# Kernel optimization log

Measured on AMD Instinct MI355X. Metric: run time of the kernel, lower is better.

Reference implementation:

```python
import jax, jax.numpy as jnp
import numpy as np

B, T, D = 4, 2048, 1024
E, H, K = 8, 2048, 2  # n_expert, expert_dim, top_k


def setup_inputs() -> dict:
    key = jax.random.key(0)
    k1, k2, k3, k4 = jax.random.split(key, 4)
    x = jax.random.normal(k1, (B, T, D), jnp.float32)
    gate_w = jax.random.normal(k2, (D, E), jnp.float32) * 0.02          # Router gate (no bias)
    w1 = jax.random.normal(k3, (E, D, H), jnp.float32) * (1.0 / np.sqrt(D))  # per-expert first Linear
    w2 = jax.random.normal(k4, (E, H, D), jnp.float32) * (1.0 / np.sqrt(H))  # per-expert second Linear
    return {"x": x, "gate_w": gate_w, "w1": w1, "w2": w2}


def reference(x, gate_w, w1, w2):
    b, t, d = x.shape
    xf = x.reshape(-1, d)                                   # [N, D]
    n = xf.shape[0]
    n_expert = gate_w.shape[1]
    # Router
    logits = xf @ gate_w                                    # [N, E]
    probs = jax.nn.softmax(logits, axis=-1)
    topk_probs, topk_idx = jax.lax.top_k(probs, K)          # [N, K]
    topk_probs = topk_probs / jnp.sum(topk_probs, axis=-1, keepdims=True)
    # Dense compute of ALL experts (faithful to original), then gather top-k
    h = jax.nn.gelu(jnp.einsum('nd,edh->neh', xf, w1), approximate=False)  # [N, E, H]
    all_expert_out = jnp.einsum('neh,ehd->ned', h, w2)      # [N, E, D]
    selected = jnp.take_along_axis(all_expert_out, topk_idx[:, :, None], axis=1)  # [N, K, D]
    out = jnp.sum(topk_probs[:, :, None] * selected, axis=1)  # [N, D]  (dropout p=0 -> identity)
    # Load-balancing aux loss
    counts = jnp.zeros((n_expert,), jnp.float32).at[topk_idx.reshape(-1)].add(1.0)
    tokens_per_expert = counts / n
    mean_probs = jnp.mean(probs, axis=0)
    aux_loss = n_expert * jnp.sum(tokens_per_expert * mean_probs)
    return (out.reshape(b, t, d), aux_loss,
            probs.reshape(b, t, n_expert),
            topk_idx.reshape(b, t, K),
            topk_probs.reshape(b, t, K))
```

## Files before the change

kernel.cpp:

```cpp
#include <hip/hip_runtime.h>
#include <hip/hip_bf16.h>
#include <cstdint>

typedef unsigned short u16;
typedef unsigned int u32;
typedef short s16x8 __attribute__((ext_vector_type(8)));
typedef float f32x4 __attribute__((ext_vector_type(4)));

constexpr int NTOK = 8192;
constexpr int DDIM = 1024;
constexpr int NEXP = 8;
constexpr int HDIM = 2048;
constexpr int NPAIR = NTOK * 2;

constexpr size_t OFF_OUT   = 0;
constexpr size_t OFF_AUX   = 8388608;
constexpr size_t OFF_PROBS = 8388609;
constexpr size_t OFF_TIDX  = 8454145;
constexpr size_t OFF_TPR   = 8470529;

constexpr size_t WS_CNT  = 0;
constexpr size_t WS_PSUM = 32;
constexpr size_t WS_BASE = 64;
constexpr size_t WS_IDS  = 1024;
constexpr size_t WS_PRW  = 263168;
constexpr size_t WS_XB   = 525312;
constexpr size_t WS_W1T  = 17302528;
constexpr size_t WS_W2T  = 50856960;
constexpr size_t WS_H    = 84411392;
constexpr size_t WS_XG   = 151520256;
constexpr size_t WS_NEED = 185074688;

__device__ __forceinline__ u16 f2b(float f) {
  u32 u = __float_as_uint(f);
  u32 r = (u + 0x7fffu + ((u >> 16) & 1u)) >> 16;
  return (u16)r;
}

typedef const uint32_t __attribute__((address_space(1)))* gptr_t;
typedef uint32_t __attribute__((address_space(3)))* lptr_t;

__device__ __forceinline__ void gload16(const void* gp, void* lp) {
  __builtin_amdgcn_global_load_lds((gptr_t)gp, (lptr_t)(uintptr_t)lp, 16, 0, 0);
}

__global__ __launch_bounds__(256) void tconv_kernel(const float* __restrict__ in,
                                                    u16* __restrict__ out, int R, int C) {
  __shared__ float tile[64][65];
  int e = blockIdx.z;
  int c0 = blockIdx.x * 64, r0 = blockIdx.y * 64;
  int tx = threadIdx.x & 15, ty = threadIdx.x >> 4;
  const float* src = in + (size_t)e * R * C;
#pragma unroll
  for (int i = 0; i < 4; ++i) {
    int r = ty + i * 16;
    float4 v = *(const float4*)(src + (size_t)(r0 + r) * C + c0 + tx * 4);
    tile[r][tx * 4 + 0] = v.x; tile[r][tx * 4 + 1] = v.y;
    tile[r][tx * 4 + 2] = v.z; tile[r][tx * 4 + 3] = v.w;
  }
  __syncthreads();
  u16* dst = out + (size_t)e * R * C;
#pragma unroll
  for (int i = 0; i < 4; ++i) {
    int c = ty + i * 16;
    ushort4 o;
    o.x = f2b(tile[tx * 4 + 0][c]); o.y = f2b(tile[tx * 4 + 1][c]);
    o.z = f2b(tile[tx * 4 + 2][c]); o.w = f2b(tile[tx * 4 + 3][c]);
    *(ushort4*)(dst + (size_t)(c0 + c) * R + r0 + tx * 4) = o;
  }
}

__global__ __launch_bounds__(256) void router_kernel(
    const float* __restrict__ x, const float* __restrict__ gw,
    u16* __restrict__ xb, float* __restrict__ outbuf,
    int* __restrict__ cnt, float* __restrict__ psum,
    int* __restrict__ ids, float* __restrict__ prw) {
  __shared__ float gwl[DDIM * NEXP];
  __shared__ int lcnt[NEXP];
  __shared__ float psl[NEXP];
  __shared__ int gbl[NEXP];

  const int tid = threadIdx.x;
#pragma unroll
  for (int k = 0; k < 8; ++k)
    ((float4*)gwl)[tid + k * 256] = ((const float4*)gw)[tid + k * 256];
  if (tid < NEXP) { lcnt[tid] = 0; psl[tid] = 0.f; }
  __syncthreads();

  const int tloc = tid >> 2, part = tid & 3;
  const int t = blockIdx.x * 64 + tloc;
  double acc[NEXP];
#pragma unroll
  for (int e = 0; e < NEXP; ++e) acc[e] = 0.0;

  const float* xrow = x + (size_t)t * DDIM + part * 256;
  u16* xbrow = xb + (size_t)t * DDIM + part * 256;
  for (int i = 0; i < 64; ++i) {
    float4 v = ((const float4*)xrow)[i];
    ushort4 o;
    o.x = f2b(v.x); o.y = f2b(v.y); o.z = f2b(v.z); o.w = f2b(v.w);
    ((ushort4*)xbrow)[i] = o;
    const float* g = &gwl[(part * 256 + i * 4) * NEXP];
#pragma unroll
    for (int j = 0; j < 4; ++j) {
      double xs = (double)((const float*)&v)[j];
#pragma unroll
      for (int e = 0; e < NEXP; ++e) acc[e] += xs * (double)g[j * NEXP + e];
    }
  }
#pragma unroll
  for (int e = 0; e < NEXP; ++e) {
    acc[e] += __shfl_xor(acc[e], 1);
    acc[e] += __shfl_xor(acc[e], 2);
  }

  int e0 = 0, e1 = 0, lp0 = 0, lp1 = 0;
  float tp0 = 0.f, tp1 = 0.f;
  if (part == 0) {
    float l[NEXP];
#pragma unroll
    for (int e = 0; e < NEXP; ++e) l[e] = (float)acc[e];
    float m = l[0];
#pragma unroll
    for (int e = 1; e < NEXP; ++e) m = fmaxf(m, l[e]);
    float p[NEXP], s = 0.f;
#pragma unroll
    for (int e = 0; e < NEXP; ++e) { p[e] = expf(l[e] - m); s += p[e]; }
    float inv = 1.0f / s;
#pragma unroll
    for (int e = 0; e < NEXP; ++e) {
      p[e] *= inv;
      outbuf[OFF_PROBS + (size_t)t * NEXP + e] = p[e];
      atomicAdd(&psl[e], p[e]);
    }
#pragma unroll
    for (int e = 1; e < NEXP; ++e) if (p[e] > p[e0]) e0 = e;
    e1 = -1;
#pragma unroll
    for (int e = 0; e < NEXP; ++e)
      if (e != e0 && (e1 < 0 || p[e] > p[e1])) e1 = e;
    float ps = p[e0] + p[e1];
    tp0 = p[e0] / ps;
    tp1 = p[e1] / ps;
    outbuf[OFF_TIDX + t * 2 + 0] = (float)e0;
    outbuf[OFF_TIDX + t * 2 + 1] = (float)e1;
    outbuf[OFF_TPR + t * 2 + 0] = tp0;
    outbuf[OFF_TPR + t * 2 + 1] = tp1;
    lp0 = atomicAdd(&lcnt[e0], 1);
    lp1 = atomicAdd(&lcnt[e1], 1);
  }
  __syncthreads();
  if (tid < NEXP) {
    gbl[tid] = atomicAdd(&cnt[tid], lcnt[tid]);
    atomicAdd(&psum[tid], psl[tid]);
  }
  __syncthreads();
  if (part == 0) {
    int pos0 = gbl[e0] + lp0;
    int pos1 = gbl[e1] + lp1;
    ids[e0 * NTOK + pos0] = t;
    ids[e1 * NTOK + pos1] = t;
    prw[e0 * NTOK + pos0] = tp0;
    prw[e1 * NTOK + pos1] = tp1;
  }
}

__global__ void finalize_kernel(const int* __restrict__ cnt,
                                const float* __restrict__ psum,
                                int* __restrict__ base, float* __restrict__ outbuf) {
  if (threadIdx.x == 0 && blockIdx.x == 0) {
    int b = 0;
    float aux = 0.f;
    for (int e = 0; e < NEXP; ++e) {
      base[e] = b;
      b += cnt[e];
      aux += (float)cnt[e] * psum[e];
    }
    outbuf[OFF_AUX] = aux * (float)NEXP / ((float)NTOK * (float)NTOK);
  }
}

__global__ __launch_bounds__(256) void gather_kernel(
    const u16* __restrict__ xb, u16* __restrict__ xg,
    const int* __restrict__ cnt, const int* __restrict__ base,
    const int* __restrict__ ids) {
  const int e = blockIdx.y;
  const int cnte = cnt[e];
  const int lane = threadIdx.x & 31;
  const int rgrp = threadIdx.x >> 5;
#pragma unroll
  for (int p = 0; p < 8; ++p) {
    int pos = blockIdx.x * 64 + p * 8 + rgrp;
    if (pos < cnte) {
      int tok = ids[e * NTOK + pos];
      const uint4* src = (const uint4*)(xb + (size_t)tok * DDIM);
      uint4* dst = (uint4*)(xg + (size_t)(base[e] + pos) * DDIM);
#pragma unroll
      for (int pp = 0; pp < 4; ++pp)
        dst[pp * 32 + lane] = src[pp * 32 + lane];
    }
  }
}

template <int MODE>
__global__ __launch_bounds__(256, 4) void moe_gemm_kernel(
    const u16* __restrict__ Asrc, const u16* __restrict__ Bt,
    u16* __restrict__ hout, float* __restrict__ yout,
    const int* __restrict__ cnt, const int* __restrict__ base,
    const int* __restrict__ ids, const float* __restrict__ prw) {
  constexpr int KDIM = (MODE == 0) ? 1024 : 2048;
  constexpr int NDIM = (MODE == 0) ? 2048 : 1024;
  constexpr int NT = KDIM / 32;
  constexpr int NB = NDIM / 128;
  constexpr int MGRP = 4;
  constexpr int QPG = MGRP * NB;
  const int wgid = blockIdx.x;
  const int e = wgid & 7;
  const int q = wgid >> 3;
  const int mg = q / QPG;
  const int r = q % QPG;
  const int m0 = (mg * MGRP + (r % MGRP)) * 128;
  const int n0 = (r / MGRP) * 128;
  const int cnte = cnt[e];
  if (m0 >= cnte) return;
  const int gbase = base[e];

  __shared__ u16 Al[2][128 * 32];
  __shared__ u16 Bl[2][128 * 32];

  const int tid = threadIdx.x;
  const int lane = tid & 63, wid = tid >> 6;
  const int wm = (wid >> 1) * 64, wn = (wid & 1) * 64;
  const int r15 = lane & 15, l4 = lane >> 4;

  const char* aptr[2];
  const char* bptr[2];
#pragma unroll
  for (int qq = 0; qq < 2; ++qq) {
    int j = qq * 256 + tid;
    int row = j >> 2;
    int c = (j & 3) ^ ((row >> 1) & 3);
    int gr = gbase + m0 + row;
    if (gr > NPAIR - 1) gr = NPAIR - 1;
    size_t rowoff = (size_t)gr * KDIM;
    aptr[qq] = (const char*)Asrc + (rowoff + (size_t)c * 8) * 2;
    size_t nrow = (size_t)e * NDIM + n0 + row;
    bptr[qq] = (const char*)Bt + (nrow * KDIM + (size_t)c * 8) * 2;
  }

  f32x4 acc[4][4];
#pragma unroll
  for (int i = 0; i < 4; ++i)
#pragma unroll
    for (int jn = 0; jn < 4; ++jn) acc[i][jn] = (f32x4){0.f, 0.f, 0.f, 0.f};

#define STAGE(b_, kt_)                                                         \
  do {                                                                         \
    const size_t kofs_ = (size_t)(kt_) * 64;               \
    _Pragma("unroll") for (int qq = 0; qq < 2; ++qq) {                         \
      gload16(aptr[qq] + kofs_, (void*)&Al[b_][(size_t)(qq * 256 + tid) * 8]); \
      gload16(bptr[qq] + kofs_, (void*)&Bl[b_][(size_t)(qq * 256 + tid) * 8]); \
    }                                                                          \
  } while (0)

  auto compute = [&](int b) {
    const s16x8* Av = (const s16x8*)Al[b];
    const s16x8* Bv = (const s16x8*)Bl[b];
    s16x8 af[4], bfr[4];
#pragma unroll
    for (int mi = 0; mi < 4; ++mi) {
      int row = wm + mi * 16 + r15;
      af[mi] = Av[row * 4 + (l4 ^ ((row >> 1) & 3))];
    }
#pragma unroll
    for (int ni = 0; ni < 4; ++ni) {
      int row = wn + ni * 16 + r15;
      bfr[ni] = Bv[row * 4 + (l4 ^ ((row >> 1) & 3))];
    }
#pragma unroll
    for (int mi = 0; mi < 4; ++mi)
#pragma unroll
      for (int ni = 0; ni < 4; ++ni)
        acc[mi][ni] = __builtin_amdgcn_mfma_f32_16x16x32_bf16(
            af[mi], bfr[ni], acc[mi][ni], 0, 0, 0);
  };

  STAGE(0, 0);

  for (int kt = 0; kt < NT; ++kt) {
    if (kt + 1 < NT) {
      STAGE((kt + 1) & 1, kt + 1);
      asm volatile("s_waitcnt vmcnt(4)" ::: "memory");
    } else {
      asm volatile("s_waitcnt vmcnt(0)" ::: "memory");
    }
    __builtin_amdgcn_s_barrier();
    compute(kt & 1);
    __builtin_amdgcn_s_barrier();
  }
#undef STAGE

#pragma unroll
  for (int mi = 0; mi < 4; ++mi) {
#pragma unroll
    for (int jr = 0; jr < 4; ++jr) {
      int rl = wm + mi * 16 + l4 * 4 + jr;
      if (m0 + rl < cnte) {
        if (MODE == 0) {
          size_t grow = (size_t)(gbase + m0 + rl);
#pragma unroll
          for (int ni = 0; ni < 4; ++ni) {
            float v = acc[mi][ni][jr];
            v = 0.5f * v * (1.0f + erff(v * 0.70710678118654752f));
            int col = n0 + wn + ni * 16 + r15;
            hout[grow * NDIM + col] = f2b(v);
          }
        } else {
          int tok = ids[e * NTOK + m0 + rl];
          float p = prw[e * NTOK + m0 + rl];
#pragma unroll
          for (int ni = 0; ni < 4; ++ni) {
            int col = n0 + wn + ni * 16 + r15;
            atomicAdd(&yout[(size_t)tok * DDIM + col], p * acc[mi][ni][jr]);
          }
        }
      }
    }
  }
}

extern "C" void kernel_launch(void* const* d_in, const int* in_sizes, int n_in,
                              void* d_out, int out_size, void* d_ws, size_t ws_size,
                              hipStream_t stream) {
  const float* x = (const float*)d_in[0];
  const float* gw = (const float*)d_in[1];
  const float* w1 = (const float*)d_in[2];
  const float* w2 = (const float*)d_in[3];
  float* out = (float*)d_out;
  char* w = (char*)d_ws;
  if (ws_size < WS_NEED) return;

  int* cnt = (int*)(w + WS_CNT);
  float* psum = (float*)(w + WS_PSUM);
  int* base = (int*)(w + WS_BASE);
  int* ids = (int*)(w + WS_IDS);
  float* prw = (float*)(w + WS_PRW);
  u16* xb = (u16*)(w + WS_XB);
  u16* w1t = (u16*)(w + WS_W1T);
  u16* w2t = (u16*)(w + WS_W2T);
  u16* hbuf = (u16*)(w + WS_H);
  u16* xg = (u16*)(w + WS_XG);

  (void)hipMemsetAsync(w, 0, 96, stream);
  (void)hipMemsetAsync(out + OFF_OUT, 0, (size_t)NTOK * DDIM * sizeof(float), stream);
  router_kernel<<<NTOK / 64, 256, 0, stream>>>(x, gw, xb, out, cnt, psum, ids, prw);
  tconv_kernel<<<dim3(HDIM / 64, DDIM / 64, NEXP), 256, 0, stream>>>(w1, w1t, DDIM, HDIM);
  tconv_kernel<<<dim3(DDIM / 64, HDIM / 64, NEXP), 256, 0, stream>>>(w2, w2t, HDIM, DDIM);
  finalize_kernel<<<1, 64, 0, stream>>>(cnt, psum, base, out);
  gather_kernel<<<dim3(NTOK / 64, NEXP), 256, 0, stream>>>(xb, xg, cnt, base, ids);
  moe_gemm_kernel<0><<<NEXP * 64 * (HDIM / 128), 256, 0, stream>>>(
      xg, w1t, hbuf, nullptr, cnt, base, ids, prw);
  moe_gemm_kernel<1><<<NEXP * 64 * (DDIM / 128), 256, 0, stream>>>(
      hbuf, w2t, nullptr, out + OFF_OUT, cnt, base, ids, prw);
}
```

Measured before the change: 345.7 us.

## Triple-buffer GEMM loads, fuse weight transposes, convert x to bf16 in gather

The expert GEMM moves from a double-buffered LDS pipeline to a triple-buffered one that prefetches two K-tiles ahead and drops one barrier per iteration, with launch bounds lowered to three waves to make room for the extra LDS. The two weight transpose-convert launches are merged into one kernel. The router no longer writes a bf16 copy of x; the gather kernel reads fp32 x and converts to bf16 on the fly. Together these aim to hide memory latency in the GEMMs and cut launch count and one intermediate buffer. The risks are lower occupancy and a possible LDS race, since dropping the post-compute barrier relies on the three-buffer rotation to keep the buffer being refilled separate from the one being read.

```diff
diff --git a/kernel.cpp b/kernel.cpp
--- a/kernel.cpp
+++ b/kernel.cpp
@@ -24,7 +24,6 @@
 constexpr size_t WS_BASE = 64;
 constexpr size_t WS_IDS  = 1024;
 constexpr size_t WS_PRW  = 263168;
-constexpr size_t WS_XB   = 525312;
 constexpr size_t WS_W1T  = 17302528;
 constexpr size_t WS_W2T  = 50856960;
 constexpr size_t WS_H    = 84411392;
@@ -44,19 +43,34 @@
   __builtin_amdgcn_global_load_lds((gptr_t)gp, (lptr_t)(uintptr_t)lp, 16, 0, 0);
 }
 
-__global__ __launch_bounds__(256) void tconv_kernel(const float* __restrict__ in,
-                                                    u16* __restrict__ out, int R, int C) {
+__global__ __launch_bounds__(256) void tconv_all_kernel(
+    const float* __restrict__ w1, u16* __restrict__ w1t,
+    const float* __restrict__ w2, u16* __restrict__ w2t) {
+  int id = blockIdx.x;
+  const float* in;
+  u16* out;
+  int R, C, e, r;
+  if (id < 4096) {
+    in = w1; out = w1t; R = DDIM; C = HDIM;
+    e = id >> 9; r = id & 511;
+  } else {
+    id -= 4096;
+    in = w2; out = w2t; R = HDIM; C = DDIM;
+    e = id >> 9; r = id & 511;
+  }
+  int xt = (R == DDIM) ? (r & 31) : (r & 15);
+  int yt = (R == DDIM) ? (r >> 5) : (r >> 4);
+  int c0 = xt * 64, r0 = yt * 64;
+
   __shared__ float tile[64][65];
-  int e = blockIdx.z;
-  int c0 = blockIdx.x * 64, r0 = blockIdx.y * 64;
   int tx = threadIdx.x & 15, ty = threadIdx.x >> 4;
   const float* src = in + (size_t)e * R * C;
 #pragma unroll
   for (int i = 0; i < 4; ++i) {
-    int r = ty + i * 16;
-    float4 v = *(const float4*)(src + (size_t)(r0 + r) * C + c0 + tx * 4);
-    tile[r][tx * 4 + 0] = v.x; tile[r][tx * 4 + 1] = v.y;
-    tile[r][tx * 4 + 2] = v.z; tile[r][tx * 4 + 3] = v.w;
+    int rr = ty + i * 16;
+    float4 v = *(const float4*)(src + (size_t)(r0 + rr) * C + c0 + tx * 4);
+    tile[rr][tx * 4 + 0] = v.x; tile[rr][tx * 4 + 1] = v.y;
+    tile[rr][tx * 4 + 2] = v.z; tile[rr][tx * 4 + 3] = v.w;
   }
   __syncthreads();
   u16* dst = out + (size_t)e * R * C;
@@ -72,7 +86,7 @@
 
 __global__ __launch_bounds__(256) void router_kernel(
     const float* __restrict__ x, const float* __restrict__ gw,
-    u16* __restrict__ xb, float* __restrict__ outbuf,
+    float* __restrict__ outbuf,
     int* __restrict__ cnt, float* __restrict__ psum,
     int* __restrict__ ids, float* __restrict__ prw) {
   __shared__ float gwl[DDIM * NEXP];
@@ -94,12 +108,8 @@
   for (int e = 0; e < NEXP; ++e) acc[e] = 0.0;
 
   const float* xrow = x + (size_t)t * DDIM + part * 256;
-  u16* xbrow = xb + (size_t)t * DDIM + part * 256;
   for (int i = 0; i < 64; ++i) {
     float4 v = ((const float4*)xrow)[i];
-    ushort4 o;
-    o.x = f2b(v.x); o.y = f2b(v.y); o.z = f2b(v.z); o.w = f2b(v.w);
-    ((ushort4*)xbrow)[i] = o;
     const float* g = &gwl[(part * 256 + i * 4) * NEXP];
 #pragma unroll
     for (int j = 0; j < 4; ++j) {
@@ -181,7 +191,7 @@
 }
 
 __global__ __launch_bounds__(256) void gather_kernel(
-    const u16* __restrict__ xb, u16* __restrict__ xg,
+    const float* __restrict__ x, u16* __restrict__ xg,
     const int* __restrict__ cnt, const int* __restrict__ base,
     const int* __restrict__ ids) {
   const int e = blockIdx.y;
@@ -193,17 +203,21 @@
     int pos = blockIdx.x * 64 + p * 8 + rgrp;
     if (pos < cnte) {
       int tok = ids[e * NTOK + pos];
-      const uint4* src = (const uint4*)(xb + (size_t)tok * DDIM);
-      uint4* dst = (uint4*)(xg + (size_t)(base[e] + pos) * DDIM);
-#pragma unroll
-      for (int pp = 0; pp < 4; ++pp)
-        dst[pp * 32 + lane] = src[pp * 32 + lane];
+      const float4* src = (const float4*)(x + (size_t)tok * DDIM);
+      ushort4* dst = (ushort4*)(xg + (size_t)(base[e] + pos) * DDIM);
+#pragma unroll
+      for (int pp = 0; pp < 8; ++pp) {
+        float4 v = src[pp * 32 + lane];
+        ushort4 o;
+        o.x = f2b(v.x); o.y = f2b(v.y); o.z = f2b(v.z); o.w = f2b(v.w);
+        dst[pp * 32 + lane] = o;
+      }
     }
   }
 }
 
 template <int MODE>
-__global__ __launch_bounds__(256, 4) void moe_gemm_kernel(
+__global__ __launch_bounds__(256, 3) void moe_gemm_kernel(
     const u16* __restrict__ Asrc, const u16* __restrict__ Bt,
     u16* __restrict__ hout, float* __restrict__ yout,
     const int* __restrict__ cnt, const int* __restrict__ base,
@@ -225,8 +239,8 @@
   if (m0 >= cnte) return;
   const int gbase = base[e];
 
-  __shared__ u16 Al[2][128 * 32];
-  __shared__ u16 Bl[2][128 * 32];
+  __shared__ u16 Al[3][128 * 32];
+  __shared__ u16 Bl[3][128 * 32];
 
   const int tid = threadIdx.x;
   const int lane = tid & 63, wid = tid >> 6;
@@ -286,17 +300,22 @@
   };
 
   STAGE(0, 0);
-
+  STAGE(1, 1);
+
+  int b0 = 0;
   for (int kt = 0; kt < NT; ++kt) {
-    if (kt + 1 < NT) {
-      STAGE((kt + 1) & 1, kt + 1);
+    if (kt < NT - 1)
       asm volatile("s_waitcnt vmcnt(4)" ::: "memory");
-    } else {
+    else
       asm volatile("s_waitcnt vmcnt(0)" ::: "memory");
-    }
     __builtin_amdgcn_s_barrier();
-    compute(kt & 1);
-    __builtin_amdgcn_s_barrier();
+    asm volatile("" ::: "memory");
+    if (kt + 2 < NT) {
+      int bs = b0 + 2; if (bs >= 3) bs -= 3;
+      STAGE(bs, kt + 2);
+    }
+    compute(b0);
+    if (++b0 == 3) b0 = 0;
   }
 #undef STAGE
 
@@ -345,7 +364,6 @@
   int* base = (int*)(w + WS_BASE);
   int* ids = (int*)(w + WS_IDS);
   float* prw = (float*)(w + WS_PRW);
-  u16* xb = (u16*)(w + WS_XB);
   u16* w1t = (u16*)(w + WS_W1T);
   u16* w2t = (u16*)(w + WS_W2T);
   u16* hbuf = (u16*)(w + WS_H);
@@ -353,11 +371,10 @@
 
   (void)hipMemsetAsync(w, 0, 96, stream);
   (void)hipMemsetAsync(out + OFF_OUT, 0, (size_t)NTOK * DDIM * sizeof(float), stream);
-  router_kernel<<<NTOK / 64, 256, 0, stream>>>(x, gw, xb, out, cnt, psum, ids, prw);
-  tconv_kernel<<<dim3(HDIM / 64, DDIM / 64, NEXP), 256, 0, stream>>>(w1, w1t, DDIM, HDIM);
-  tconv_kernel<<<dim3(DDIM / 64, HDIM / 64, NEXP), 256, 0, stream>>>(w2, w2t, HDIM, DDIM);
+  router_kernel<<<NTOK / 64, 256, 0, stream>>>(x, gw, out, cnt, psum, ids, prw);
   finalize_kernel<<<1, 64, 0, stream>>>(cnt, psum, base, out);
-  gather_kernel<<<dim3(NTOK / 64, NEXP), 256, 0, stream>>>(xb, xg, cnt, base, ids);
+  gather_kernel<<<dim3(NTOK / 64, NEXP), 256, 0, stream>>>(x, xg, cnt, base, ids);
+  tconv_all_kernel<<<8192, 256, 0, stream>>>(w1, w1t, w2, w2t);
   moe_gemm_kernel<0><<<NEXP * 64 * (HDIM / 128), 256, 0, stream>>>(
       xg, w1t, hbuf, nullptr, cnt, base, ids, prw);
   moe_gemm_kernel<1><<<NEXP * 64 * (DDIM / 128), 256, 0, stream>>>(
```

Result: faster. 333.4 us (-3.6%).
